# Kernel tuning notes

Measured on AMD Instinct MI355X. Metric: run time of the kernel, lower is better.

Reference implementation:

```python
import jax, jax.numpy as jnp
import numpy as np

TAU = 2.0       # spikingjelly LIFNode default
V_TH = 1.0      # v_threshold default
ALPHA = 2.0     # surrogate.ATan default alpha

@jax.custom_vjp
def atan_spike(x):
    # Heaviside forward, ATan surrogate gradient backward
    return (x >= 0.0).astype(x.dtype)

def _atan_fwd(x):
    return atan_spike(x), x

def _atan_bwd(x, g):
    return (g * (ALPHA / 2.0) / (1.0 + (jnp.pi / 2.0 * ALPHA * x) ** 2),)

atan_spike.defvjp(_atan_fwd, _atan_bwd)

def lif_scan(cur):
    # cur: [T, ...]; LIF with decay_input=True, hard reset to v_reset=0
    def step(v, c):
        v = v + (c - v) / TAU          # charge with decayed input
        s = atan_spike(v - V_TH)       # fire
        v = (1.0 - s) * v              # hard reset (v_reset = 0)
        return v, s
    v0 = jnp.zeros(cur.shape[1:], cur.dtype)
    _, spikes = jax.lax.scan(step, v0, cur)
    return spikes

def setup_inputs() -> dict:
    key = jax.random.key(0)
    k1, k2 = jax.random.split(key, 2)
    T, B, D = 2048, 32, 512
    x = jax.random.normal(k1, (T, B, D), dtype=jnp.float32)
    W = jax.random.normal(k2, (D, D), dtype=jnp.float32) / np.sqrt(D).astype(np.float32)
    b = jnp.zeros((D,), dtype=jnp.float32)
    return {"x": x, "W": W, "b": b}

def reference(x, W, b):
    # x: [T, B, D]
    xs = jnp.stack([x, jnp.flip(x, axis=0)], axis=2)          # [T, B, 2, D]
    cur = jnp.einsum('tbkd,ed->tbke', xs, W) + b              # Linear (y = x W^T + b)
    s = lif_scan(cur)                                          # [T, B, 2, D] spikes
    return s[:, :, 0, :] + jnp.flip(s[:, :, 1, :], axis=0)    # [T, B, D]
```

## Files before the change

### kernel.cpp

```cpp
#include <hip/hip_runtime.h>
#include <cstddef>
#include <cstdint>

#define T_LEN 2048
#define B_SZ  32
#define D_SZ  512
#define BD    (B_SZ * D_SZ)

#define BM  128
#define BN  128
#define LDP 20

__global__ __launch_bounds__(256) void gemm8x8_kernel(
    const float* __restrict__ A,
    const float* __restrict__ W,
    const float* __restrict__ bias,
    float* __restrict__ Y)
{
#pragma clang fp contract(off)
  __shared__ float As[BM][LDP];
  __shared__ float Bs[BN][LDP];

  const int tid = threadIdx.x;
  const int tx  = tid & 15;
  const int ty  = tid >> 4;
  const int m0  = blockIdx.x * BM;
  const int n0  = blockIdx.y * BN;

  const int sr = tid >> 2;
  const int sq = (tid & 3) << 2;

  const float* Ap0 = A + (size_t)(m0 + sr)      * D_SZ + sq;
  const float* Ap1 = A + (size_t)(m0 + 64 + sr) * D_SZ + sq;
  const float* Wp0 = W + (size_t)(n0 + sr)      * D_SZ + sq;
  const float* Wp1 = W + (size_t)(n0 + 64 + sr) * D_SZ + sq;

  float acc[8][8];
#pragma unroll
  for (int i = 0; i < 8; ++i)
#pragma unroll
    for (int j = 0; j < 8; ++j) acc[i][j] = 0.0f;

  float4 pa0 = *(const float4*)(Ap0);
  float4 pa1 = *(const float4*)(Ap1);
  float4 pb0 = *(const float4*)(Wp0);
  float4 pb1 = *(const float4*)(Wp1);

#pragma unroll 1
  for (int k0 = 0; k0 < D_SZ; k0 += 16) {
    __syncthreads();
    *(float4*)&As[sr][sq]      = pa0;
    *(float4*)&As[64 + sr][sq] = pa1;
    *(float4*)&Bs[sr][sq]      = pb0;
    *(float4*)&Bs[64 + sr][sq] = pb1;
    __syncthreads();

    if (k0 + 16 < D_SZ) {
      pa0 = *(const float4*)(Ap0 + k0 + 16);
      pa1 = *(const float4*)(Ap1 + k0 + 16);
      pb0 = *(const float4*)(Wp0 + k0 + 16);
      pb1 = *(const float4*)(Wp1 + k0 + 16);
    }

#pragma unroll
    for (int kq = 0; kq < 4; ++kq) {
      float4 b[8];
#pragma unroll
      for (int j = 0; j < 8; ++j)
        b[j] = *(const float4*)&Bs[tx + 16 * j][kq << 2];
#pragma unroll
      for (int i = 0; i < 8; ++i) {
        const float4 a = *(const float4*)&As[ty + 16 * i][kq << 2];
#pragma unroll
        for (int j = 0; j < 8; ++j) {
          acc[i][j] = fmaf(a.x, b[j].x, acc[i][j]);
          acc[i][j] = fmaf(a.y, b[j].y, acc[i][j]);
          acc[i][j] = fmaf(a.z, b[j].z, acc[i][j]);
          acc[i][j] = fmaf(a.w, b[j].w, acc[i][j]);
        }
      }
    }
  }

#pragma unroll
  for (int i = 0; i < 8; ++i) {
    const int m = m0 + ty + 16 * i;
#pragma unroll
    for (int j = 0; j < 8; ++j) {
      const int n = n0 + tx + 16 * j;
      Y[(size_t)m * D_SZ + n] = acc[i][j] + bias[n];
    }
  }
}

__global__ __launch_bounds__(64) void scan_dirs_kernel(
    const float* __restrict__ Y,
    uint32_t* __restrict__ bits_f,
    uint32_t* __restrict__ bits_b)
{
#pragma clang fp contract(off)
  const int blk = blockIdx.x;
  const bool fwd = blk < 256;
  const int idx = ((fwd ? blk : blk - 256) << 6) + threadIdx.x;
  float v = 0.0f;

  if (fwd) {
#pragma unroll 1
    for (int g = 0; g < 64; ++g) {
      float c[32];
#pragma unroll
      for (int j = 0; j < 32; ++j)
        c[j] = Y[(size_t)(g * 32 + j) * BD + idx];
      uint32_t w = 0;
#pragma unroll
      for (int j = 0; j < 32; ++j) {
        v = v + (c[j] - v) * 0.5f;
        const bool s = (v - 1.0f) >= 0.0f;
        w |= (uint32_t)s << j;
        v = s ? 0.0f : v;
      }
      bits_f[g * BD + idx] = w;
    }
  } else {
#pragma unroll 1
    for (int g = 63; g >= 0; --g) {
      float c[32];
#pragma unroll
      for (int j = 0; j < 32; ++j)
        c[j] = Y[(size_t)(g * 32 + j) * BD + idx];
      uint32_t w = 0;
#pragma unroll
      for (int j = 31; j >= 0; --j) {
        v = v + (c[j] - v) * 0.5f;
        const bool s = (v - 1.0f) >= 0.0f;
        w |= (uint32_t)s << j;
        v = s ? 0.0f : v;
      }
      bits_b[g * BD + idx] = w;
    }
  }
}

__global__ __launch_bounds__(256) void combine_kernel(
    const uint32_t* __restrict__ bf,
    const uint32_t* __restrict__ bb,
    float* __restrict__ out)
{
  const int gid = blockIdx.x * 256 + threadIdx.x;
  const int f0  = gid << 2;
  const int t   = f0 / BD;
  const int i0  = f0 & (BD - 1);
  const int g   = t >> 5;
  const int bit = t & 31;
  const uint4 wf = *(const uint4*)(bf + g * BD + i0);
  const uint4 wb = *(const uint4*)(bb + g * BD + i0);
  float4 r;
  r.x = (float)(((wf.x >> bit) & 1u) + ((wb.x >> bit) & 1u));
  r.y = (float)(((wf.y >> bit) & 1u) + ((wb.y >> bit) & 1u));
  r.z = (float)(((wf.z >> bit) & 1u) + ((wb.z >> bit) & 1u));
  r.w = (float)(((wf.w >> bit) & 1u) + ((wb.w >> bit) & 1u));
  *(float4*)(out + (size_t)f0) = r;
}

__global__ __launch_bounds__(64) void lif_fwd_kernel(
    const float* __restrict__ Y, float* __restrict__ out,
    int tlen, float* __restrict__ vstate, int carry)
{
#pragma clang fp contract(off)
  const int idx = blockIdx.x * 64 + threadIdx.x;
  float v = carry ? vstate[idx] : 0.0f;
#pragma unroll 16
  for (int t = 0; t < tlen; ++t) {
    const float c = Y[(size_t)t * BD + idx];
    v = v + (c - v) * 0.5f;
    const bool s = (v - 1.0f) >= 0.0f;
    out[(size_t)t * BD + idx] = s ? 1.0f : 0.0f;
    v = s ? 0.0f : v;
  }
  vstate[idx] = v;
}

__global__ __launch_bounds__(64) void lif_bwd_kernel(
    const float* __restrict__ Y, float* __restrict__ out,
    int tlen, float* __restrict__ vstate, int carry)
{
#pragma clang fp contract(off)
  const int idx = blockIdx.x * 64 + threadIdx.x;
  float v = carry ? vstate[idx] : 0.0f;
#pragma unroll 16
  for (int tt = 0; tt < tlen; ++tt) {
    const size_t t = (size_t)(tlen - 1 - tt);
    const float c = Y[t * BD + idx];
    v = v + (c - v) * 0.5f;
    const bool s = (v - 1.0f) >= 0.0f;
    out[t * BD + idx] += s ? 1.0f : 0.0f;
    v = s ? 0.0f : v;
  }
  vstate[idx] = v;
}

extern "C" void kernel_launch(void* const* d_in, const int* in_sizes, int n_in,
                              void* d_out, int out_size, void* d_ws, size_t ws_size,
                              hipStream_t stream)
{
  const float* x = (const float*)d_in[0];
  const float* W = (const float*)d_in[1];
  const float* b = (const float*)d_in[2];
  float* out = (float*)d_out;

  const size_t full_bytes = (size_t)T_LEN * BD * sizeof(float);
  const size_t bit_bytes  = (size_t)(T_LEN / 32) * BD * sizeof(uint32_t);
  const size_t vbytes     = (size_t)BD * sizeof(float);

  if (ws_size >= full_bytes + 2 * bit_bytes) {
    float*    Y  = (float*)d_ws;
    uint32_t* bf = (uint32_t*)((char*)d_ws + full_bytes);
    uint32_t* bb = (uint32_t*)((char*)d_ws + full_bytes + bit_bytes);
    dim3 grid(T_LEN * B_SZ / BM, D_SZ / BN);
    gemm8x8_kernel<<<grid, 256, 0, stream>>>(x, W, b, Y);
    scan_dirs_kernel<<<512, 64, 0, stream>>>(Y, bf, bb);
    combine_kernel<<<(T_LEN * BD / 4) / 256, 256, 0, stream>>>(bf, bb, out);
  } else if (ws_size >= full_bytes + vbytes) {
    float* Y      = (float*)d_ws;
    float* vstate = (float*)((char*)d_ws + full_bytes);
    dim3 grid(T_LEN * B_SZ / BM, D_SZ / BN);
    gemm8x8_kernel<<<grid, 256, 0, stream>>>(x, W, b, Y);
    lif_fwd_kernel<<<BD / 64, 64, 0, stream>>>(Y, out, T_LEN, vstate, 0);
    lif_bwd_kernel<<<BD / 64, 64, 0, stream>>>(Y, out, T_LEN, vstate, 0);
  } else {
    const size_t avail = ws_size > vbytes ? ws_size - vbytes : 0;
    int Tc = T_LEN;
    while (Tc > 4 && (size_t)Tc * BD * sizeof(float) > avail) Tc >>= 1;
    float* Y      = (float*)d_ws;
    float* vstate = (float*)((char*)d_ws + (size_t)Tc * BD * sizeof(float));

    int first = 1;
    for (int t0 = 0; t0 < T_LEN; t0 += Tc) {
      dim3 grid(Tc * B_SZ / BM, D_SZ / BN);
      gemm8x8_kernel<<<grid, 256, 0, stream>>>(x + (size_t)t0 * BD, W, b, Y);
      lif_fwd_kernel<<<BD / 64, 64, 0, stream>>>(Y, out + (size_t)t0 * BD, Tc,
                                                 vstate, first ? 0 : 1);
      first = 0;
    }
    first = 1;
    for (int t0 = T_LEN - Tc; t0 >= 0; t0 -= Tc) {
      dim3 grid(Tc * B_SZ / BM, D_SZ / BN);
      gemm8x8_kernel<<<grid, 256, 0, stream>>>(x + (size_t)t0 * BD, W, b, Y);
      lif_bwd_kernel<<<BD / 64, 64, 0, stream>>>(Y, out + (size_t)t0 * BD, Tc,
                                                 vstate, first ? 0 : 1);
      first = 0;
    }
  }
}
```

Baseline: 712.7 us.

## Enlarge GEMM tile to 16x8 per thread and double-buffer scan loads

The GEMM block tile grows from 128 to 256 rows, so each thread computes a 16x8 output micro-tile. This raises arithmetic intensity per shared-memory load, at the cost of 128 accumulators per thread (launch bounds now request 2 blocks per SM) and half as many blocks. The scan kernel now prefetches the next 32-step chunk of currents into a second register buffer while it processes the current chunk, to hide global load latency on the serial recurrence. The extra register pressure risks spills or lower occupancy.

```diff
diff --git a/kernel.cpp b/kernel.cpp
--- a/kernel.cpp
+++ b/kernel.cpp
@@ -7,11 +7,11 @@
 #define D_SZ  512
 #define BD    (B_SZ * D_SZ)
 
-#define BM  128
+#define BM  256
 #define BN  128
 #define LDP 20
 
-__global__ __launch_bounds__(256) void gemm8x8_kernel(
+__global__ __launch_bounds__(256, 2) void gemm16x8_kernel(
     const float* __restrict__ A,
     const float* __restrict__ W,
     const float* __restrict__ bias,
@@ -30,34 +30,42 @@
   const int sr = tid >> 2;
   const int sq = (tid & 3) << 2;
 
-  const float* Ap0 = A + (size_t)(m0 + sr)      * D_SZ + sq;
-  const float* Ap1 = A + (size_t)(m0 + 64 + sr) * D_SZ + sq;
-  const float* Wp0 = W + (size_t)(n0 + sr)      * D_SZ + sq;
-  const float* Wp1 = W + (size_t)(n0 + 64 + sr) * D_SZ + sq;
-
-  float acc[8][8];
-#pragma unroll
-  for (int i = 0; i < 8; ++i)
+  const float* Ap0 = A + (size_t)(m0 + sr)       * D_SZ + sq;
+  const float* Ap1 = A + (size_t)(m0 + 64 + sr)  * D_SZ + sq;
+  const float* Ap2 = A + (size_t)(m0 + 128 + sr) * D_SZ + sq;
+  const float* Ap3 = A + (size_t)(m0 + 192 + sr) * D_SZ + sq;
+  const float* Wp0 = W + (size_t)(n0 + sr)       * D_SZ + sq;
+  const float* Wp1 = W + (size_t)(n0 + 64 + sr)  * D_SZ + sq;
+
+  float acc[16][8];
+#pragma unroll
+  for (int i = 0; i < 16; ++i)
 #pragma unroll
     for (int j = 0; j < 8; ++j) acc[i][j] = 0.0f;
 
   float4 pa0 = *(const float4*)(Ap0);
   float4 pa1 = *(const float4*)(Ap1);
+  float4 pa2 = *(const float4*)(Ap2);
+  float4 pa3 = *(const float4*)(Ap3);
   float4 pb0 = *(const float4*)(Wp0);
   float4 pb1 = *(const float4*)(Wp1);
 
 #pragma unroll 1
   for (int k0 = 0; k0 < D_SZ; k0 += 16) {
     __syncthreads();
-    *(float4*)&As[sr][sq]      = pa0;
-    *(float4*)&As[64 + sr][sq] = pa1;
-    *(float4*)&Bs[sr][sq]      = pb0;
-    *(float4*)&Bs[64 + sr][sq] = pb1;
+    *(float4*)&As[sr][sq]       = pa0;
+    *(float4*)&As[64 + sr][sq]  = pa1;
+    *(float4*)&As[128 + sr][sq] = pa2;
+    *(float4*)&As[192 + sr][sq] = pa3;
+    *(float4*)&Bs[sr][sq]       = pb0;
+    *(float4*)&Bs[64 + sr][sq]  = pb1;
     __syncthreads();
 
     if (k0 + 16 < D_SZ) {
       pa0 = *(const float4*)(Ap0 + k0 + 16);
       pa1 = *(const float4*)(Ap1 + k0 + 16);
+      pa2 = *(const float4*)(Ap2 + k0 + 16);
+      pa3 = *(const float4*)(Ap3 + k0 + 16);
       pb0 = *(const float4*)(Wp0 + k0 + 16);
       pb1 = *(const float4*)(Wp1 + k0 + 16);
     }
@@ -69,7 +77,7 @@
       for (int j = 0; j < 8; ++j)
         b[j] = *(const float4*)&Bs[tx + 16 * j][kq << 2];
 #pragma unroll
-      for (int i = 0; i < 8; ++i) {
+      for (int i = 0; i < 16; ++i) {
         const float4 a = *(const float4*)&As[ty + 16 * i][kq << 2];
 #pragma unroll
         for (int j = 0; j < 8; ++j) {
@@ -83,7 +91,7 @@
   }
 
 #pragma unroll
-  for (int i = 0; i < 8; ++i) {
+  for (int i = 0; i < 16; ++i) {
     const int m = m0 + ty + 16 * i;
 #pragma unroll
     for (int j = 0; j < 8; ++j) {
@@ -103,40 +111,71 @@
   const bool fwd = blk < 256;
   const int idx = ((fwd ? blk : blk - 256) << 6) + threadIdx.x;
   float v = 0.0f;
+  float cA[32], cB[32];
 
   if (fwd) {
+#pragma unroll
+    for (int j = 0; j < 32; ++j) cA[j] = Y[(size_t)j * BD + idx];
 #pragma unroll 1
-    for (int g = 0; g < 64; ++g) {
-      float c[32];
+    for (int g = 0; g < 64; g += 2) {
 #pragma unroll
       for (int j = 0; j < 32; ++j)
-        c[j] = Y[(size_t)(g * 32 + j) * BD + idx];
+        cB[j] = Y[(size_t)((g + 1) * 32 + j) * BD + idx];
       uint32_t w = 0;
 #pragma unroll
       for (int j = 0; j < 32; ++j) {
-        v = v + (c[j] - v) * 0.5f;
+        v = v + (cA[j] - v) * 0.5f;
         const bool s = (v - 1.0f) >= 0.0f;
         w |= (uint32_t)s << j;
         v = s ? 0.0f : v;
       }
       bits_f[g * BD + idx] = w;
+      if (g + 2 < 64) {
+#pragma unroll
+        for (int j = 0; j < 32; ++j)
+          cA[j] = Y[(size_t)((g + 2) * 32 + j) * BD + idx];
+      }
+      w = 0;
+#pragma unroll
+      for (int j = 0; j < 32; ++j) {
+        v = v + (cB[j] - v) * 0.5f;
+        const bool s = (v - 1.0f) >= 0.0f;
+        w |= (uint32_t)s << j;
+        v = s ? 0.0f : v;
+      }
+      bits_f[(g + 1) * BD + idx] = w;
     }
   } else {
+#pragma unroll
+    for (int j = 0; j < 32; ++j) cA[j] = Y[(size_t)(63 * 32 + j) * BD + idx];
 #pragma unroll 1
-    for (int g = 63; g >= 0; --g) {
-      float c[32];
+    for (int g = 63; g >= 0; g -= 2) {
 #pragma unroll
       for (int j = 0; j < 32; ++j)
-        c[j] = Y[(size_t)(g * 32 + j) * BD + idx];
+        cB[j] = Y[(size_t)((g - 1) * 32 + j) * BD + idx];
       uint32_t w = 0;
 #pragma unroll
       for (int j = 31; j >= 0; --j) {
-        v = v + (c[j] - v) * 0.5f;
+        v = v + (cA[j] - v) * 0.5f;
         const bool s = (v - 1.0f) >= 0.0f;
         w |= (uint32_t)s << j;
         v = s ? 0.0f : v;
       }
       bits_b[g * BD + idx] = w;
+      if (g - 2 >= 0) {
+#pragma unroll
+        for (int j = 0; j < 32; ++j)
+          cA[j] = Y[(size_t)((g - 2) * 32 + j) * BD + idx];
+      }
+      w = 0;
+#pragma unroll
+      for (int j = 31; j >= 0; --j) {
+        v = v + (cB[j] - v) * 0.5f;
+        const bool s = (v - 1.0f) >= 0.0f;
+        w |= (uint32_t)s << j;
+        v = s ? 0.0f : v;
+      }
+      bits_b[(g - 1) * BD + idx] = w;
     }
   }
 }
@@ -217,27 +256,27 @@
     uint32_t* bf = (uint32_t*)((char*)d_ws + full_bytes);
     uint32_t* bb = (uint32_t*)((char*)d_ws + full_bytes + bit_bytes);
     dim3 grid(T_LEN * B_SZ / BM, D_SZ / BN);
-    gemm8x8_kernel<<<grid, 256, 0, stream>>>(x, W, b, Y);
+    gemm16x8_kernel<<<grid, 256, 0, stream>>>(x, W, b, Y);
     scan_dirs_kernel<<<512, 64, 0, stream>>>(Y, bf, bb);
     combine_kernel<<<(T_LEN * BD / 4) / 256, 256, 0, stream>>>(bf, bb, out);
   } else if (ws_size >= full_bytes + vbytes) {
     float* Y      = (float*)d_ws;
     float* vstate = (float*)((char*)d_ws + full_bytes);
     dim3 grid(T_LEN * B_SZ / BM, D_SZ / BN);
-    gemm8x8_kernel<<<grid, 256, 0, stream>>>(x, W, b, Y);
+    gemm16x8_kernel<<<grid, 256, 0, stream>>>(x, W, b, Y);
     lif_fwd_kernel<<<BD / 64, 64, 0, stream>>>(Y, out, T_LEN, vstate, 0);
     lif_bwd_kernel<<<BD / 64, 64, 0, stream>>>(Y, out, T_LEN, vstate, 0);
   } else {
     const size_t avail = ws_size > vbytes ? ws_size - vbytes : 0;
     int Tc = T_LEN;
-    while (Tc > 4 && (size_t)Tc * BD * sizeof(float) > avail) Tc >>= 1;
+    while (Tc > 8 && (size_t)Tc * BD * sizeof(float) > avail) Tc >>= 1;
     float* Y      = (float*)d_ws;
     float* vstate = (float*)((char*)d_ws + (size_t)Tc * BD * sizeof(float));
 
     int first = 1;
     for (int t0 = 0; t0 < T_LEN; t0 += Tc) {
       dim3 grid(Tc * B_SZ / BM, D_SZ / BN);
-      gemm8x8_kernel<<<grid, 256, 0, stream>>>(x + (size_t)t0 * BD, W, b, Y);
+      gemm16x8_kernel<<<grid, 256, 0, stream>>>(x + (size_t)t0 * BD, W, b, Y);
       lif_fwd_kernel<<<BD / 64, 64, 0, stream>>>(Y, out + (size_t)t0 * BD, Tc,
                                                  vstate, first ? 0 : 1);
       first = 0;
@@ -245,7 +284,7 @@
     first = 1;
     for (int t0 = T_LEN - Tc; t0 >= 0; t0 -= Tc) {
       dim3 grid(Tc * B_SZ / BM, D_SZ / BN);
-      gemm8x8_kernel<<<grid, 256, 0, stream>>>(x + (size_t)t0 * BD, W, b, Y);
+      gemm16x8_kernel<<<grid, 256, 0, stream>>>(x + (size_t)t0 * BD, W, b, Y);
       lif_bwd_kernel<<<BD / 64, 64, 0, stream>>>(Y, out + (size_t)t0 * BD, Tc,
                                                  vstate, first ? 0 : 1);
       first = 0;
```

After: 1.243 ms. 74.4% more time.
